# Kernel optimization log

Hardware: AMD Instinct MI355X
Metric: run time of the kernel (lower is better)

The kernel has to match this reference:

```python
import jax, jax.numpy as jnp
import numpy as np

B, N, D = 16, 128, 128

def setup_inputs() -> dict:
    key = jax.random.key(0)
    ks = jax.random.split(key, 7)
    h = jax.random.normal(ks[0], (B, N, D), dtype=jnp.float32)
    adj = jax.random.randint(ks[1], (B, N, N), 0, 2).astype(jnp.float32)
    e = jax.random.normal(ks[2], (B, N, N, D), dtype=jnp.float32)
    # torch.nn.Linear weights: [out_features, in_features]
    Wm = jax.random.normal(ks[3], (D, 3 * D), dtype=jnp.float32) * (1.0 / np.sqrt(3 * D))
    bm = jax.random.normal(ks[4], (D,), dtype=jnp.float32) * 0.01
    Wu = jax.random.normal(ks[5], (D, 2 * D), dtype=jnp.float32) * (1.0 / np.sqrt(2 * D))
    bu = jax.random.normal(ks[6], (D,), dtype=jnp.float32) * 0.01
    return {"h": h, "adj": adj, "e": e, "Wm": Wm, "bm": bm, "Wu": Wu, "bu": bu}

def reference(h, adj, e, Wm, bm, Wu, bu):
    # Split the message Linear over the concat [h_i, h_j, e] -> three matmuls
    # (same math as cat+Linear, without materializing the [B,N,N,3D] tensor).
    d = h.shape[-1]
    W1, W2, W3 = Wm[:, :d], Wm[:, d:2 * d], Wm[:, 2 * d:]
    hi = jnp.einsum('bnd,kd->bnk', h, W1)            # sender term  [B,N,Dout]
    hj = jnp.einsum('bnd,kd->bnk', h, W2)            # receiver term [B,N,Dout]
    me = jnp.einsum('bijd,kd->bijk', e, W3)          # edge term     [B,N,N,Dout]
    m = hi[:, :, None, :] + hj[:, None, :, :] + me + bm  # [B,N,N,Dout]
    m = m * adj[..., None]                            # mask by adjacency
    m = m.sum(axis=1)                                 # sum over senders i -> [B,N,Dout]
    h_cat = jnp.concatenate([h, m], axis=2)           # [B,N,2D]
    return jnp.einsum('bnd,kd->bnk', h_cat, Wu) + bu  # [B,N,D]
```

## Files before the change

kernel.cpp:

```cpp
#include <hip/hip_runtime.h>
#include <hip/hip_bf16.h>

#define BB 16
#define NN 128
#define DD 128

typedef __attribute__((ext_vector_type(8))) short s8v;
typedef __attribute__((ext_vector_type(4))) float f4v;

__device__ __forceinline__ unsigned short f2bf(float f) {
    __hip_bfloat16 b = __float2bfloat16(f);
    return *reinterpret_cast<unsigned short*>(&b);
}

__global__ __launch_bounds__(256) void main_kernel(
    const float* __restrict__ h, const float* __restrict__ adj,
    const float* __restrict__ e, const float* __restrict__ Wm,
    const float* __restrict__ bm, const float* __restrict__ Wu,
    unsigned short* __restrict__ BT, float* __restrict__ bmWu,
    unsigned short* __restrict__ hbf, unsigned short* __restrict__ esbf,
    unsigned short* __restrict__ AHbf, float* __restrict__ deg) {
    const int bid = blockIdx.x, t = threadIdx.x;

    __shared__ float sm_big[4096];
    __shared__ float sm_adj[NN];

    if (bid < 2048) {
        const int b = bid >> 7, j = bid & 127;
        float4 (*red)[32] = (float4 (*)[32])sm_big;
        if (t < NN) sm_adj[t] = adj[(size_t)(b * NN + t) * NN + j];
        __syncthreads();
        const int d4 = t & 31, ig = t >> 5;
        const float4* __restrict__ e4 =
            (const float4*)e + ((size_t)(b * NN) * NN + j) * 32 + d4;
        const int i0 = ig * 16;
        float4 acc = make_float4(0.f, 0.f, 0.f, 0.f);
        #pragma unroll
        for (int ii = 0; ii < 16; ++ii) {
            const float a = sm_adj[i0 + ii];
            if (a != 0.0f) {
                const float4 v = e4[(size_t)(i0 + ii) * (NN * 32)];
                acc.x += a * v.x; acc.y += a * v.y;
                acc.z += a * v.z; acc.w += a * v.w;
            }
        }
        red[ig][d4] = acc;
        __syncthreads();
        if (t < 32) {
            float4 s = red[0][t];
            #pragma unroll
            for (int r = 1; r < 8; ++r) {
                const float4 v = red[r][t];
                s.x += v.x; s.y += v.y; s.z += v.z; s.w += v.w;
            }
            ((uint2*)esbf)[(size_t)bid * 32 + t] =
                make_uint2((unsigned)f2bf(s.x) | ((unsigned)f2bf(s.y) << 16),
                           (unsigned)f2bf(s.z) | ((unsigned)f2bf(s.w) << 16));
        }
    } else if (bid < 2304) {
        const int b2 = bid - 2048;
        const int b = b2 >> 4, jbase = (b2 & 15) * 8;
        float (*adj_s)[NN] = (float (*)[NN])sm_big;
        for (int x = t; x < 8 * NN; x += 256) {
            const int i = x >> 3, j2 = x & 7;
            adj_s[j2][i] = adj[(size_t)(b * NN + i) * NN + jbase + j2];
        }
        __syncthreads();
        {
            const int jj = t >> 5, l = t & 31;
            float s = adj_s[jj][l] + adj_s[jj][l + 32] + adj_s[jj][l + 64] + adj_s[jj][l + 96];
            #pragma unroll
            for (int off = 16; off; off >>= 1) s += __shfl_xor(s, off);
            if (l == 0) deg[b * NN + jbase + jj] = s;
        }
        const int k = t & 127, jh = t >> 7;
        float a0 = 0.f, a1 = 0.f, a2 = 0.f, a3 = 0.f;
        const float* __restrict__ hp = h + (size_t)b * NN * DD + k;
        #pragma unroll 8
        for (int m = 0; m < 32; ++m) {
            const float4 aA = *(const float4*)&adj_s[jh][4 * m];
            const float4 aB = *(const float4*)&adj_s[jh + 2][4 * m];
            const float4 aC = *(const float4*)&adj_s[jh + 4][4 * m];
            const float4 aD = *(const float4*)&adj_s[jh + 6][4 * m];
            const float h0 = hp[(size_t)(4 * m + 0) * DD];
            const float h1 = hp[(size_t)(4 * m + 1) * DD];
            const float h2 = hp[(size_t)(4 * m + 2) * DD];
            const float h3 = hp[(size_t)(4 * m + 3) * DD];
            a0 += aA.x * h0 + aA.y * h1 + aA.z * h2 + aA.w * h3;
            a1 += aB.x * h0 + aB.y * h1 + aB.z * h2 + aB.w * h3;
            a2 += aC.x * h0 + aC.y * h1 + aC.z * h2 + aC.w * h3;
            a3 += aD.x * h0 + aD.y * h1 + aD.z * h2 + aD.w * h3;
        }
        AHbf[(size_t)(b * NN + jbase + jh) * DD + k]     = f2bf(a0);
        AHbf[(size_t)(b * NN + jbase + jh + 2) * DD + k] = f2bf(a1);
        AHbf[(size_t)(b * NN + jbase + jh + 4) * DD + k] = f2bf(a2);
        AHbf[(size_t)(b * NN + jbase + jh + 6) * DD + k] = f2bf(a3);
    } else if (bid < 2352) {
        float* chunk = sm_big;
        const int g = bid - 2304;
        const int m = g >> 4, dc = g & 15;
        const int off   = (m == 0) ? 0   : (m == 1) ? 256 : 128;
        const int rbase = (m == 0) ? 128 : (m == 1) ? 256 : 384;
        const int k = t & 127, dh = t >> 7;
        const int d0 = dc * 8 + dh * 4;
        float a0 = 0, a1 = 0, a2 = 0, a3 = 0;
        for (int c = 0; c < 4; ++c) {
            for (int x = t; x < 32 * 128; x += 256) {
                const int kk = x >> 7, kcol = x & 127;
                chunk[kk * 128 + kcol] = Wu[kcol * 256 + 128 + c * 32 + kk];
            }
            __syncthreads();
            #pragma unroll 8
            for (int kk = 0; kk < 32; ++kk) {
                const float wu = chunk[kk * 128 + k];
                const float* wmp = Wm + (c * 32 + kk) * 384 + off + d0;
                a0 += wmp[0] * wu; a1 += wmp[1] * wu;
                a2 += wmp[2] * wu; a3 += wmp[3] * wu;
            }
            __syncthreads();
        }
        unsigned short* bp = BT + (size_t)k * 512 + rbase + d0;
        bp[0] = f2bf(a0); bp[1] = f2bf(a1); bp[2] = f2bf(a2); bp[3] = f2bf(a3);
    } else if (bid == 2352) {
        for (int p = 0; p < 64; ++p) {
            const int x = p * 256 + t, k = x >> 7, d = x & 127;
            BT[(size_t)k * 512 + d] = f2bf(Wu[k * 256 + d]);
        }
        if (t < 128) {
            float s = 0.f;
            for (int kk = 0; kk < 128; ++kk) s += bm[kk] * Wu[t * 256 + 128 + kk];
            bmWu[t] = s;
        }
    } else {
        const int bi = bid - 2353;
        const float4* h4 = (const float4*)h;
        uint2* hb2 = (uint2*)hbf;
        for (int p = 0; p < 32; ++p) {
            const int i4 = bi * 8192 + p * 256 + t;
            const float4 v = h4[i4];
            hb2[i4] = make_uint2((unsigned)f2bf(v.x) | ((unsigned)f2bf(v.y) << 16),
                                 (unsigned)f2bf(v.z) | ((unsigned)f2bf(v.w) << 16));
        }
    }
}

__global__ __launch_bounds__(256) void out_kernel(
    const unsigned short* __restrict__ hbf, const unsigned short* __restrict__ AHbf,
    const unsigned short* __restrict__ esbf, const unsigned short* __restrict__ BT,
    const float* __restrict__ deg, const float* __restrict__ bmWu,
    const float* __restrict__ bu, float* __restrict__ out) {
    const int rt = blockIdx.x >> 2, ct = blockIdx.x & 3;
    const int t = threadIdx.x;
    const int l = t & 63, wid = t >> 6, mw = wid >> 1, nw = wid & 1;
    __shared__ unsigned short A_s[32][72], B_s[32][72], B2_s[32][72];
    f4v acc1 = {0.f, 0.f, 0.f, 0.f};
    f4v acc2 = {0.f, 0.f, 0.f, 0.f};
    const int rA = t >> 3, cb = t & 7;
    const int arow = mw * 16 + (l & 15);
    const int brow = nw * 16 + (l & 15);
    const int lg = l >> 4;
    for (int c = 0; c < 6; ++c) {
        __syncthreads();
        const unsigned short* src = (c < 2) ? hbf : (c < 4) ? AHbf : esbf;
        const int col0 = (c & 1) * 64;
        const int rowg = rt * 32 + rA;
        *(s8v*)&A_s[rA][cb * 8] = *(const s8v*)&src[(size_t)rowg * 128 + col0 + cb * 8];
        *(s8v*)&B_s[rA][cb * 8] =
            *(const s8v*)&BT[(size_t)(ct * 32 + rA) * 512 + c * 64 + cb * 8];
        if (c < 2)
            *(s8v*)&B2_s[rA][cb * 8] =
                *(const s8v*)&BT[(size_t)(ct * 32 + rA) * 512 + 384 + c * 64 + cb * 8];
        __syncthreads();
        #pragma unroll
        for (int kit = 0; kit < 2; ++kit) {
            const s8v a  = *(const s8v*)&A_s[arow][kit * 32 + lg * 8];
            const s8v bb = *(const s8v*)&B_s[brow][kit * 32 + lg * 8];
            acc1 = __builtin_amdgcn_mfma_f32_16x16x32_bf16(a, bb, acc1, 0, 0, 0);
            if (c < 2) {
                const s8v b2 = *(const s8v*)&B2_s[brow][kit * 32 + lg * 8];
                acc2 = __builtin_amdgcn_mfma_f32_16x16x32_bf16(a, b2, acc2, 0, 0, 0);
            }
        }
    }
    const int colk = ct * 32 + nw * 16 + (l & 15);
    const float bmv = bmWu[colk], buv = bu[colk];
    #pragma unroll
    for (int r = 0; r < 4; ++r) {
        const int rowg = rt * 32 + mw * 16 + (l >> 4) * 4 + r;
        const float dg = deg[rowg];
        out[(size_t)rowg * 128 + colk] = acc1[r] + dg * acc2[r] + dg * bmv + buv;
    }
}

extern "C" void kernel_launch(void* const* d_in, const int* in_sizes, int n_in,
                              void* d_out, int out_size, void* d_ws, size_t ws_size,
                              hipStream_t stream) {
    const float* h   = (const float*)d_in[0];
    const float* adj = (const float*)d_in[1];
    const float* e   = (const float*)d_in[2];
    const float* Wm  = (const float*)d_in[3];
    const float* bm  = (const float*)d_in[4];
    const float* Wu  = (const float*)d_in[5];
    const float* bu  = (const float*)d_in[6];
    float* out = (float*)d_out;

    float* ws = (float*)d_ws;
    unsigned short* BT   = (unsigned short*)ws;
    float*          bmWu = ws + 32768;
    float*          deg  = ws + 32896;
    unsigned short* hbf  = (unsigned short*)(ws + 34944);
    unsigned short* AHbf = (unsigned short*)(ws + 166016);
    unsigned short* esbf = (unsigned short*)(ws + 297088);

    main_kernel<<<2361, 256, 0, stream>>>(h, adj, e, Wm, bm, Wu,
                                          BT, bmWu, hbf, esbf, AHbf, deg);
    out_kernel<<<256, 256, 0, stream>>>(hbf, AHbf, esbf, BT, deg, bmWu, bu, out);
}
```

Baseline: 38.69 us.

## Compact nonzero adjacency indices and reorder blocks so small jobs launch first

After: 34.37 us. 1.13x faster.

```diff
diff --git a/kernel.cpp b/kernel.cpp
--- a/kernel.cpp
+++ b/kernel.cpp
@@ -13,7 +13,7 @@
     return *reinterpret_cast<unsigned short*>(&b);
 }
 
-__global__ __launch_bounds__(256) void main_kernel(
+__global__ __launch_bounds__(256) void front_kernel(
     const float* __restrict__ h, const float* __restrict__ adj,
     const float* __restrict__ e, const float* __restrict__ Wm,
     const float* __restrict__ bm, const float* __restrict__ Wu,
@@ -24,41 +24,57 @@
 
     __shared__ float sm_big[4096];
     __shared__ float sm_adj[NN];
-
-    if (bid < 2048) {
-        const int b = bid >> 7, j = bid & 127;
-        float4 (*red)[32] = (float4 (*)[32])sm_big;
-        if (t < NN) sm_adj[t] = adj[(size_t)(b * NN + t) * NN + j];
-        __syncthreads();
-        const int d4 = t & 31, ig = t >> 5;
-        const float4* __restrict__ e4 =
-            (const float4*)e + ((size_t)(b * NN) * NN + j) * 32 + d4;
-        const int i0 = ig * 16;
-        float4 acc = make_float4(0.f, 0.f, 0.f, 0.f);
-        #pragma unroll
-        for (int ii = 0; ii < 16; ++ii) {
-            const float a = sm_adj[i0 + ii];
-            if (a != 0.0f) {
-                const float4 v = e4[(size_t)(i0 + ii) * (NN * 32)];
-                acc.x += a * v.x; acc.y += a * v.y;
-                acc.z += a * v.z; acc.w += a * v.w;
-            }
-        }
-        red[ig][d4] = acc;
-        __syncthreads();
-        if (t < 32) {
-            float4 s = red[0][t];
-            #pragma unroll
-            for (int r = 1; r < 8; ++r) {
-                const float4 v = red[r][t];
-                s.x += v.x; s.y += v.y; s.z += v.z; s.w += v.w;
-            }
-            ((uint2*)esbf)[(size_t)bid * 32 + t] =
-                make_uint2((unsigned)f2bf(s.x) | ((unsigned)f2bf(s.y) << 16),
-                           (unsigned)f2bf(s.z) | ((unsigned)f2bf(s.w) << 16));
-        }
-    } else if (bid < 2304) {
-        const int b2 = bid - 2048;
+    __shared__ int   sm_idx[NN];
+    __shared__ float sm_av[NN];
+    __shared__ int   sm_cnt;
+
+    if (bid < 48) {
+        float* chunk = sm_big;
+        const int m = bid >> 4, dc = bid & 15;
+        const int off   = (m == 0) ? 0   : (m == 1) ? 256 : 128;
+        const int rbase = (m == 0) ? 128 : (m == 1) ? 256 : 384;
+        const int k = t & 127, dh = t >> 7;
+        const int d0 = dc * 8 + dh * 4;
+        float a0 = 0, a1 = 0, a2 = 0, a3 = 0;
+        for (int c = 0; c < 4; ++c) {
+            for (int x = t; x < 32 * 128; x += 256) {
+                const int kk = x >> 7, kcol = x & 127;
+                chunk[kk * 128 + kcol] = Wu[kcol * 256 + 128 + c * 32 + kk];
+            }
+            __syncthreads();
+            #pragma unroll 8
+            for (int kk = 0; kk < 32; ++kk) {
+                const float wu = chunk[kk * 128 + k];
+                const float* wmp = Wm + (c * 32 + kk) * 384 + off + d0;
+                a0 += wmp[0] * wu; a1 += wmp[1] * wu;
+                a2 += wmp[2] * wu; a3 += wmp[3] * wu;
+            }
+            __syncthreads();
+        }
+        unsigned short* bp = BT + (size_t)k * 512 + rbase + d0;
+        bp[0] = f2bf(a0); bp[1] = f2bf(a1); bp[2] = f2bf(a2); bp[3] = f2bf(a3);
+    } else if (bid == 48) {
+        for (int p = 0; p < 64; ++p) {
+            const int x = p * 256 + t, k = x >> 7, d = x & 127;
+            BT[(size_t)k * 512 + d] = f2bf(Wu[k * 256 + d]);
+        }
+        if (t < 128) {
+            float s = 0.f;
+            for (int kk = 0; kk < 128; ++kk) s += bm[kk] * Wu[t * 256 + 128 + kk];
+            bmWu[t] = s;
+        }
+    } else if (bid < 57) {
+        const int bi = bid - 49;
+        const float4* h4 = (const float4*)h;
+        uint2* hb2 = (uint2*)hbf;
+        for (int p = 0; p < 32; ++p) {
+            const int i4 = bi * 8192 + p * 256 + t;
+            const float4 v = h4[i4];
+            hb2[i4] = make_uint2((unsigned)f2bf(v.x) | ((unsigned)f2bf(v.y) << 16),
+                                 (unsigned)f2bf(v.z) | ((unsigned)f2bf(v.w) << 16));
+        }
+    } else if (bid < 313) {
+        const int b2 = bid - 57;
         const int b = b2 >> 4, jbase = (b2 & 15) * 8;
         float (*adj_s)[NN] = (float (*)[NN])sm_big;
         for (int x = t; x < 8 * NN; x += 256) {
@@ -95,51 +111,60 @@
         AHbf[(size_t)(b * NN + jbase + jh + 2) * DD + k] = f2bf(a1);
         AHbf[(size_t)(b * NN + jbase + jh + 4) * DD + k] = f2bf(a2);
         AHbf[(size_t)(b * NN + jbase + jh + 6) * DD + k] = f2bf(a3);
-    } else if (bid < 2352) {
-        float* chunk = sm_big;
-        const int g = bid - 2304;
-        const int m = g >> 4, dc = g & 15;
-        const int off   = (m == 0) ? 0   : (m == 1) ? 256 : 128;
-        const int rbase = (m == 0) ? 128 : (m == 1) ? 256 : 384;
-        const int k = t & 127, dh = t >> 7;
-        const int d0 = dc * 8 + dh * 4;
-        float a0 = 0, a1 = 0, a2 = 0, a3 = 0;
-        for (int c = 0; c < 4; ++c) {
-            for (int x = t; x < 32 * 128; x += 256) {
-                const int kk = x >> 7, kcol = x & 127;
-                chunk[kk * 128 + kcol] = Wu[kcol * 256 + 128 + c * 32 + kk];
-            }
-            __syncthreads();
-            #pragma unroll 8
-            for (int kk = 0; kk < 32; ++kk) {
-                const float wu = chunk[kk * 128 + k];
-                const float* wmp = Wm + (c * 32 + kk) * 384 + off + d0;
-                a0 += wmp[0] * wu; a1 += wmp[1] * wu;
-                a2 += wmp[2] * wu; a3 += wmp[3] * wu;
-            }
-            __syncthreads();
-        }
-        unsigned short* bp = BT + (size_t)k * 512 + rbase + d0;
-        bp[0] = f2bf(a0); bp[1] = f2bf(a1); bp[2] = f2bf(a2); bp[3] = f2bf(a3);
-    } else if (bid == 2352) {
-        for (int p = 0; p < 64; ++p) {
-            const int x = p * 256 + t, k = x >> 7, d = x & 127;
-            BT[(size_t)k * 512 + d] = f2bf(Wu[k * 256 + d]);
-        }
-        if (t < 128) {
-            float s = 0.f;
-            for (int kk = 0; kk < 128; ++kk) s += bm[kk] * Wu[t * 256 + 128 + kk];
-            bmWu[t] = s;
-        }
     } else {
-        const int bi = bid - 2353;
-        const float4* h4 = (const float4*)h;
-        uint2* hb2 = (uint2*)hbf;
-        for (int p = 0; p < 32; ++p) {
-            const int i4 = bi * 8192 + p * 256 + t;
-            const float4 v = h4[i4];
-            hb2[i4] = make_uint2((unsigned)f2bf(v.x) | ((unsigned)f2bf(v.y) << 16),
-                                 (unsigned)f2bf(v.z) | ((unsigned)f2bf(v.w) << 16));
+        const int bj = bid - 313;
+        const int b = bj >> 7, j = bj & 127;
+        float4 (*red)[32] = (float4 (*)[32])sm_big;
+        if (t < NN) sm_adj[t] = adj[(size_t)(b * NN + t) * NN + j];
+        __syncthreads();
+        if (t < 64) {
+            const float a0 = sm_adj[t], a1 = sm_adj[t + 64];
+            const unsigned long long m0 = __ballot(a0 != 0.0f);
+            const unsigned long long m1 = __ballot(a1 != 0.0f);
+            const int c0 = __popcll(m0);
+            const unsigned long long below = (t == 0) ? 0ull : ((1ull << t) - 1ull);
+            const int p0 = __popcll(m0 & below);
+            const int p1 = c0 + __popcll(m1 & below);
+            if (a0 != 0.0f) { sm_idx[p0] = t;      sm_av[p0] = a0; }
+            if (a1 != 0.0f) { sm_idx[p1] = t + 64; sm_av[p1] = a1; }
+            const int cnt = c0 + __popcll(m1);
+            const int cntP = (cnt + 31) & ~31;
+            for (int x = cnt + t; x < cntP; x += 64) { sm_idx[x] = 0; sm_av[x] = 0.f; }
+            if (t == 0) sm_cnt = cntP;
+        }
+        __syncthreads();
+        const int cnt = sm_cnt;
+        const int d4 = t & 31, g = t >> 5;
+        const float4* __restrict__ ep =
+            (const float4*)e + ((size_t)(b * NN) * NN + j) * 32 + d4;
+        f4v acc = {0.f, 0.f, 0.f, 0.f};
+        for (int base = 0; base < cnt; base += 32) {
+            const int n = base + g;
+            const int   iA = sm_idx[n];      const float aA = sm_av[n];
+            const int   iB = sm_idx[n + 8];  const float aB = sm_av[n + 8];
+            const int   iC = sm_idx[n + 16]; const float aC = sm_av[n + 16];
+            const int   iD = sm_idx[n + 24]; const float aD = sm_av[n + 24];
+            const float4 vA = ep[(size_t)iA * (NN * 32)];
+            const float4 vB = ep[(size_t)iB * (NN * 32)];
+            const float4 vC = ep[(size_t)iC * (NN * 32)];
+            const float4 vD = ep[(size_t)iD * (NN * 32)];
+            acc.x += aA * vA.x + aB * vB.x + aC * vC.x + aD * vD.x;
+            acc.y += aA * vA.y + aB * vB.y + aC * vC.y + aD * vD.y;
+            acc.z += aA * vA.z + aB * vB.z + aC * vC.z + aD * vD.z;
+            acc.w += aA * vA.w + aB * vB.w + aC * vC.w + aD * vD.w;
+        }
+        red[g][d4] = make_float4(acc.x, acc.y, acc.z, acc.w);
+        __syncthreads();
+        if (t < 32) {
+            float4 s = red[0][t];
+            #pragma unroll
+            for (int r = 1; r < 8; ++r) {
+                const float4 v = red[r][t];
+                s.x += v.x; s.y += v.y; s.z += v.z; s.w += v.w;
+            }
+            ((uint2*)esbf)[(size_t)bj * 32 + t] =
+                make_uint2((unsigned)f2bf(s.x) | ((unsigned)f2bf(s.y) << 16),
+                           (unsigned)f2bf(s.z) | ((unsigned)f2bf(s.w) << 16));
         }
     }
 }
@@ -212,7 +237,7 @@
     unsigned short* AHbf = (unsigned short*)(ws + 166016);
     unsigned short* esbf = (unsigned short*)(ws + 297088);
 
-    main_kernel<<<2361, 256, 0, stream>>>(h, adj, e, Wm, bm, Wu,
-                                          BT, bmWu, hbf, esbf, AHbf, deg);
+    front_kernel<<<313 + BB * NN, 256, 0, stream>>>(h, adj, e, Wm, bm, Wu,
+                                                    BT, bmWu, hbf, esbf, AHbf, deg);
     out_kernel<<<256, 256, 0, stream>>>(hbf, AHbf, esbf, BT, deg, bmWu, bu, out);
 }
```

## Reorder fused prep blocks and process two edge columns per block without branching

Applied to the files above, without the earlier changes.

New measurement: 42.58 us. 10.1% more time.

```diff
diff --git a/kernel.cpp b/kernel.cpp
--- a/kernel.cpp
+++ b/kernel.cpp
@@ -13,7 +13,7 @@
     return *reinterpret_cast<unsigned short*>(&b);
 }
 
-__global__ __launch_bounds__(256) void main_kernel(
+__global__ __launch_bounds__(256) void front_kernel(
     const float* __restrict__ h, const float* __restrict__ adj,
     const float* __restrict__ e, const float* __restrict__ Wm,
     const float* __restrict__ bm, const float* __restrict__ Wu,
@@ -23,82 +23,10 @@
     const int bid = blockIdx.x, t = threadIdx.x;
 
     __shared__ float sm_big[4096];
-    __shared__ float sm_adj[NN];
-
-    if (bid < 2048) {
-        const int b = bid >> 7, j = bid & 127;
-        float4 (*red)[32] = (float4 (*)[32])sm_big;
-        if (t < NN) sm_adj[t] = adj[(size_t)(b * NN + t) * NN + j];
-        __syncthreads();
-        const int d4 = t & 31, ig = t >> 5;
-        const float4* __restrict__ e4 =
-            (const float4*)e + ((size_t)(b * NN) * NN + j) * 32 + d4;
-        const int i0 = ig * 16;
-        float4 acc = make_float4(0.f, 0.f, 0.f, 0.f);
-        #pragma unroll
-        for (int ii = 0; ii < 16; ++ii) {
-            const float a = sm_adj[i0 + ii];
-            if (a != 0.0f) {
-                const float4 v = e4[(size_t)(i0 + ii) * (NN * 32)];
-                acc.x += a * v.x; acc.y += a * v.y;
-                acc.z += a * v.z; acc.w += a * v.w;
-            }
-        }
-        red[ig][d4] = acc;
-        __syncthreads();
-        if (t < 32) {
-            float4 s = red[0][t];
-            #pragma unroll
-            for (int r = 1; r < 8; ++r) {
-                const float4 v = red[r][t];
-                s.x += v.x; s.y += v.y; s.z += v.z; s.w += v.w;
-            }
-            ((uint2*)esbf)[(size_t)bid * 32 + t] =
-                make_uint2((unsigned)f2bf(s.x) | ((unsigned)f2bf(s.y) << 16),
-                           (unsigned)f2bf(s.z) | ((unsigned)f2bf(s.w) << 16));
-        }
-    } else if (bid < 2304) {
-        const int b2 = bid - 2048;
-        const int b = b2 >> 4, jbase = (b2 & 15) * 8;
-        float (*adj_s)[NN] = (float (*)[NN])sm_big;
-        for (int x = t; x < 8 * NN; x += 256) {
-            const int i = x >> 3, j2 = x & 7;
-            adj_s[j2][i] = adj[(size_t)(b * NN + i) * NN + jbase + j2];
-        }
-        __syncthreads();
-        {
-            const int jj = t >> 5, l = t & 31;
-            float s = adj_s[jj][l] + adj_s[jj][l + 32] + adj_s[jj][l + 64] + adj_s[jj][l + 96];
-            #pragma unroll
-            for (int off = 16; off; off >>= 1) s += __shfl_xor(s, off);
-            if (l == 0) deg[b * NN + jbase + jj] = s;
-        }
-        const int k = t & 127, jh = t >> 7;
-        float a0 = 0.f, a1 = 0.f, a2 = 0.f, a3 = 0.f;
-        const float* __restrict__ hp = h + (size_t)b * NN * DD + k;
-        #pragma unroll 8
-        for (int m = 0; m < 32; ++m) {
-            const float4 aA = *(const float4*)&adj_s[jh][4 * m];
-            const float4 aB = *(const float4*)&adj_s[jh + 2][4 * m];
-            const float4 aC = *(const float4*)&adj_s[jh + 4][4 * m];
-            const float4 aD = *(const float4*)&adj_s[jh + 6][4 * m];
-            const float h0 = hp[(size_t)(4 * m + 0) * DD];
-            const float h1 = hp[(size_t)(4 * m + 1) * DD];
-            const float h2 = hp[(size_t)(4 * m + 2) * DD];
-            const float h3 = hp[(size_t)(4 * m + 3) * DD];
-            a0 += aA.x * h0 + aA.y * h1 + aA.z * h2 + aA.w * h3;
-            a1 += aB.x * h0 + aB.y * h1 + aB.z * h2 + aB.w * h3;
-            a2 += aC.x * h0 + aC.y * h1 + aC.z * h2 + aC.w * h3;
-            a3 += aD.x * h0 + aD.y * h1 + aD.z * h2 + aD.w * h3;
-        }
-        AHbf[(size_t)(b * NN + jbase + jh) * DD + k]     = f2bf(a0);
-        AHbf[(size_t)(b * NN + jbase + jh + 2) * DD + k] = f2bf(a1);
-        AHbf[(size_t)(b * NN + jbase + jh + 4) * DD + k] = f2bf(a2);
-        AHbf[(size_t)(b * NN + jbase + jh + 6) * DD + k] = f2bf(a3);
-    } else if (bid < 2352) {
+
+    if (bid < 48) {
         float* chunk = sm_big;
-        const int g = bid - 2304;
-        const int m = g >> 4, dc = g & 15;
+        const int m = bid >> 4, dc = bid & 15;
         const int off   = (m == 0) ? 0   : (m == 1) ? 256 : 128;
         const int rbase = (m == 0) ? 128 : (m == 1) ? 256 : 384;
         const int k = t & 127, dh = t >> 7;
@@ -121,7 +49,7 @@
         }
         unsigned short* bp = BT + (size_t)k * 512 + rbase + d0;
         bp[0] = f2bf(a0); bp[1] = f2bf(a1); bp[2] = f2bf(a2); bp[3] = f2bf(a3);
-    } else if (bid == 2352) {
+    } else if (bid == 48) {
         for (int p = 0; p < 64; ++p) {
             const int x = p * 256 + t, k = x >> 7, d = x & 127;
             BT[(size_t)k * 512 + d] = f2bf(Wu[k * 256 + d]);
@@ -131,8 +59,8 @@
             for (int kk = 0; kk < 128; ++kk) s += bm[kk] * Wu[t * 256 + 128 + kk];
             bmWu[t] = s;
         }
-    } else {
-        const int bi = bid - 2353;
+    } else if (bid < 57) {
+        const int bi = bid - 49;
         const float4* h4 = (const float4*)h;
         uint2* hb2 = (uint2*)hbf;
         for (int p = 0; p < 32; ++p) {
@@ -140,6 +68,80 @@
             const float4 v = h4[i4];
             hb2[i4] = make_uint2((unsigned)f2bf(v.x) | ((unsigned)f2bf(v.y) << 16),
                                  (unsigned)f2bf(v.z) | ((unsigned)f2bf(v.w) << 16));
+        }
+    } else if (bid < 313) {
+        const int b2 = bid - 57;
+        const int b = b2 >> 4, jbase = (b2 & 15) * 8;
+        float (*adj_s)[NN] = (float (*)[NN])sm_big;
+        for (int x = t; x < 8 * NN; x += 256) {
+            const int i = x >> 3, j2 = x & 7;
+            adj_s[j2][i] = adj[(size_t)(b * NN + i) * NN + jbase + j2];
+        }
+        __syncthreads();
+        {
+            const int jj = t >> 5, l = t & 31;
+            float s = adj_s[jj][l] + adj_s[jj][l + 32] + adj_s[jj][l + 64] + adj_s[jj][l + 96];
+            #pragma unroll
+            for (int off = 16; off; off >>= 1) s += __shfl_xor(s, off);
+            if (l == 0) deg[b * NN + jbase + jj] = s;
+        }
+        const int k = t & 127, jh = t >> 7;
+        float a0 = 0.f, a1 = 0.f, a2 = 0.f, a3 = 0.f;
+        const float* __restrict__ hp = h + (size_t)b * NN * DD + k;
+        #pragma unroll 8
+        for (int m = 0; m < 32; ++m) {
+            const float4 aA = *(const float4*)&adj_s[jh][4 * m];
+            const float4 aB = *(const float4*)&adj_s[jh + 2][4 * m];
+            const float4 aC = *(const float4*)&adj_s[jh + 4][4 * m];
+            const float4 aD = *(const float4*)&adj_s[jh + 6][4 * m];
+            const float h0 = hp[(size_t)(4 * m + 0) * DD];
+            const float h1 = hp[(size_t)(4 * m + 1) * DD];
+            const float h2 = hp[(size_t)(4 * m + 2) * DD];
+            const float h3 = hp[(size_t)(4 * m + 3) * DD];
+            a0 += aA.x * h0 + aA.y * h1 + aA.z * h2 + aA.w * h3;
+            a1 += aB.x * h0 + aB.y * h1 + aB.z * h2 + aB.w * h3;
+            a2 += aC.x * h0 + aC.y * h1 + aC.z * h2 + aC.w * h3;
+            a3 += aD.x * h0 + aD.y * h1 + aD.z * h2 + aD.w * h3;
+        }
+        AHbf[(size_t)(b * NN + jbase + jh) * DD + k]     = f2bf(a0);
+        AHbf[(size_t)(b * NN + jbase + jh + 2) * DD + k] = f2bf(a1);
+        AHbf[(size_t)(b * NN + jbase + jh + 4) * DD + k] = f2bf(a2);
+        AHbf[(size_t)(b * NN + jbase + jh + 6) * DD + k] = f2bf(a3);
+    } else {
+        const int bjp = bid - 313;
+        const int b = bjp >> 6, j0 = (bjp & 63) * 2;
+        float  (*adj2)[2] = (float (*)[2])sm_big;
+        float4* red2 = (float4*)(sm_big + 256);
+        if (t < 256) {
+            const int i = t >> 1, jc = t & 1;
+            adj2[i][jc] = adj[(size_t)(b * NN + i) * NN + j0 + jc];
+        }
+        __syncthreads();
+        const int w = t >> 6, l = t & 63;
+        const int jsel = l >> 5, d4 = l & 31;
+        const float4* __restrict__ ep =
+            (const float4*)e + ((size_t)(b * NN) * NN + j0 + jsel) * 32 + d4;
+        f4v acc = {0.f, 0.f, 0.f, 0.f};
+        #pragma unroll 4
+        for (int m = 0; m < 32; ++m) {
+            const int i = 4 * m + w;
+            const float a = adj2[i][jsel];
+            const float4 v = ep[(size_t)i * (NN * 32)];
+            acc.x += a * v.x; acc.y += a * v.y;
+            acc.z += a * v.z; acc.w += a * v.w;
+        }
+        red2[w * 64 + l] = make_float4(acc.x, acc.y, acc.z, acc.w);
+        __syncthreads();
+        if (t < 64) {
+            const float4 s0 = red2[t], s1 = red2[64 + t];
+            const float4 s2 = red2[128 + t], s3 = red2[192 + t];
+            const float sx = s0.x + s1.x + s2.x + s3.x;
+            const float sy = s0.y + s1.y + s2.y + s3.y;
+            const float sz = s0.z + s1.z + s2.z + s3.z;
+            const float sw = s0.w + s1.w + s2.w + s3.w;
+            ((uint2*)esbf)[((size_t)(b * NN + j0 + (t >> 5))) * 32 + (t & 31)] =
+                make_uint2((unsigned)f2bf(sx) | ((unsigned)f2bf(sy) << 16),
+                           (unsigned)f2bf(sz) | ((unsigned)f2bf(sw) << 16));
         }
     }
 }
@@ -212,7 +214,7 @@
     unsigned short* AHbf = (unsigned short*)(ws + 166016);
     unsigned short* esbf = (unsigned short*)(ws + 297088);
 
-    main_kernel<<<2361, 256, 0, stream>>>(h, adj, e, Wm, bm, Wu,
-                                          BT, bmWu, hbf, esbf, AHbf, deg);
+    front_kernel<<<313 + 1024, 256, 0, stream>>>(h, adj, e, Wm, bm, Wu,
+                                                 BT, bmWu, hbf, esbf, AHbf, deg);
     out_kernel<<<256, 256, 0, stream>>>(hbf, AHbf, esbf, BT, deg, bmWu, bu, out);
 }
```
